# Kernel tuning notes

Measured on AMD Instinct MI355X. Metric: run time of the kernel, lower is better.

Reference implementation:

```python
import jax, jax.numpy as jnp
import numpy as np

B, C, HF, WF = 64, 512, 28, 28
HID = 512
NUM_CLS = 30
LOC_REG = 8
MAX_LEN = 500  # loop runs MAX_LEN + 1 = 501 steps


def setup_inputs() -> dict:
    key = jax.random.key(0)
    ks = jax.random.split(key, 12)
    sc = 0.02
    rn = lambda k, shape: jax.random.normal(k, shape, jnp.float32) * sc
    z = lambda shape: jnp.zeros(shape, jnp.float32)
    return {
        "fea": jax.random.normal(ks[0], (B, C, HF, WF), jnp.float32),
        # AttentionGRUCell params
        "i2h_w": rn(ks[1], (HID, C)),            # Linear(C, H, bias=False)
        "h2h_w": rn(ks[2], (HID, HID)),
        "h2h_b": z((HID,)),
        "score_w": rn(ks[3], (1, HID)),          # Linear(H, 1, bias=False)
        "gru_w_ih": rn(ks[4], (3 * HID, C + NUM_CLS)),
        "gru_w_hh": rn(ks[5], (3 * HID, HID)),
        "gru_b_ih": z((3 * HID,)),
        "gru_b_hh": z((3 * HID,)),
        # structure_generator: Linear(H,H) -> Linear(H, NUM_CLS) (no activation)
        "sg1_w": rn(ks[6], (HID, HID)), "sg1_b": z((HID,)),
        "sg2_w": rn(ks[7], (NUM_CLS, HID)), "sg2_b": z((NUM_CLS,)),
        # loc_generator: Linear(H,H) -> Linear(H, LOC_REG) -> Sigmoid
        "lg1_w": rn(ks[8], (HID, HID)), "lg1_b": z((HID,)),
        "lg2_w": rn(ks[9], (LOC_REG, HID)), "lg2_b": z((LOC_REG,)),
    }


def reference(fea, i2h_w, h2h_w, h2h_b, score_w, gru_w_ih, gru_w_hh,
              gru_b_ih, gru_b_hh, sg1_w, sg1_b, sg2_w, sg2_b,
              lg1_w, lg1_b, lg2_w, lg2_b):
    b = fea.shape[0]
    feat = fea.reshape(b, fea.shape[1], -1).transpose(0, 2, 1)      # [B, T, C]
    # i2h(batch_H) is step-invariant: hoist it out of the decode loop
    feat_proj = jnp.einsum('btc,hc->bth', feat, i2h_w)              # [B, T, H]
    sv = score_w[0]                                                  # [H]

    def gru_cell(x, h):
        gi = x @ gru_w_ih.T + gru_b_ih
        gh = h @ gru_w_hh.T + gru_b_hh
        i_r, i_z, i_n = jnp.split(gi, 3, axis=-1)
        h_r, h_z, h_n = jnp.split(gh, 3, axis=-1)
        r = jax.nn.sigmoid(i_r + h_r)
        z = jax.nn.sigmoid(i_z + h_z)
        n = jnp.tanh(i_n + r * h_n)
        return (1.0 - z) * n + z * h

    def step(carry, _):
        hidden, pre_chars = carry
        onehot = jax.nn.one_hot(pre_chars, NUM_CLS, dtype=feat.dtype)
        hproj = hidden @ h2h_w.T + h2h_b                             # [B, H]
        e = jnp.einsum('bth,h->bt', jnp.tanh(feat_proj + hproj[:, None, :]), sv)
        alpha = jax.nn.softmax(e, axis=1)                            # [B, T]
        context = jnp.einsum('bt,btc->bc', alpha, feat)              # [B, C]
        x = jnp.concatenate([context, onehot], axis=1)               # [B, C+NUM_CLS]
        new_hidden = gru_cell(x, hidden)
        structure_step = (new_hidden @ sg1_w.T + sg1_b) @ sg2_w.T + sg2_b
        loc_step = jax.nn.sigmoid((new_hidden @ lg1_w.T + lg1_b) @ lg2_w.T + lg2_b)
        new_chars = jnp.argmax(structure_step, axis=1)               # greedy decode
        return (new_hidden, new_chars), (structure_step, loc_step)

    hidden0 = jnp.zeros((b, HID), feat.dtype)
    chars0 = jnp.zeros((b,), jnp.int32)
    _, (structs, locs) = jax.lax.scan(step, (hidden0, chars0), None, length=MAX_LEN + 1)
    structure_probs = jax.nn.softmax(structs.transpose(1, 0, 2), axis=-1)  # eval-mode softmax
    loc_preds = locs.transpose(1, 0, 2)
    return structure_probs, loc_preds
```

## Files before the change

### kernel.cpp

```cpp
#include <hip/hip_runtime.h>
#include <hip/hip_bf16.h>


#define NB 64
#define TT 784
#define CC 512
#define HH 512
#define NCLS 30
#define LREG 8
#define STEPS 501
#define GRID_MAIN 256
#define THR_MAIN 1024
#define LROWS 52

struct SlaP {
  __hip_bfloat16* feat16;
  __hip_bfloat16* fp16;
  float* hid2;
  float* hproj;
  float* h1sg;
  float* h1lg;
  float* ctx2;
  float* wsum;
  int*   chars;
  unsigned* bar;
  const float *score_w, *w_ih, *w_hh, *b_ih, *b_hh;
  const float *h2h_w, *h2h_b, *sg1_w, *sg1_b, *sg2_w, *sg2_b;
  const float *lg1_w, *lg1_b, *lg2_w, *lg2_b;
  float *out_probs, *out_loc;
};

__device__ __forceinline__ float lo16(unsigned v){ return __uint_as_float(v << 16); }
__device__ __forceinline__ float hi16(unsigned v){ return __uint_as_float(v & 0xffff0000u); }

__device__ __forceinline__ float cld(const float* p){
  return __hip_atomic_load(p, __ATOMIC_RELAXED, __HIP_MEMORY_SCOPE_AGENT);
}
__device__ __forceinline__ void cst(float* p, float v){
  __hip_atomic_store(p, v, __ATOMIC_RELAXED, __HIP_MEMORY_SCOPE_AGENT);
}
__device__ __forceinline__ int cldi(const int* p){
  return __hip_atomic_load(p, __ATOMIC_RELAXED, __HIP_MEMORY_SCOPE_AGENT);
}
__device__ __forceinline__ void csti(int* p, int v){
  __hip_atomic_store(p, v, __ATOMIC_RELAXED, __HIP_MEMORY_SCOPE_AGENT);
}
__device__ __forceinline__ float2 cld2(const float* p){
  unsigned long long v = __hip_atomic_load((const unsigned long long*)p,
                          __ATOMIC_RELAXED, __HIP_MEMORY_SCOPE_AGENT);
  union { unsigned long long u; float2 f; } c; c.u = v; return c.f;
}
__device__ __forceinline__ void cst2(float* p, float a, float b){
  union { unsigned long long u; float2 f; } c; c.f = make_float2(a, b);
  __hip_atomic_store((unsigned long long*)p, c.u,
                     __ATOMIC_RELAXED, __HIP_MEMORY_SCOPE_AGENT);
}

__device__ __forceinline__ float tanh_fast(float x){
  float ex = __expf(2.f * x);
  return 1.f - 2.f * __builtin_amdgcn_rcpf(ex + 1.f);
}
__device__ __forceinline__ float sigmoid_fast(float x){
  return __builtin_amdgcn_rcpf(1.f + __expf(-x));
}
__device__ __forceinline__ float warp_sum(float v){
  #pragma unroll
  for (int m = 32; m > 0; m >>= 1) v += __shfl_xor(v, m, 64);
  return v;
}
__device__ __forceinline__ float warp_max(float v){
  #pragma unroll
  for (int m = 32; m > 0; m >>= 1) v = fmaxf(v, __shfl_xor(v, m, 64));
  return v;
}
__device__ __forceinline__ int warp_min_i(int v){
  #pragma unroll
  for (int m = 32; m > 0; m >>= 1) v = min(v, __shfl_xor(v, m, 64));
  return v;
}

__device__ __forceinline__ void att_quad(const uint4* f, const uint4* g, int count,
                                         const float* hpr, const float* svr,
                                         float* acc, float& wsr){
  float e[4];
  #pragma unroll
  for (int j = 0; j < 4; ++j){
    float s = 0.f, x;
    x = lo16(f[j].x)+hpr[0]; s += tanh_fast(x)*svr[0];
    x = hi16(f[j].x)+hpr[1]; s += tanh_fast(x)*svr[1];
    x = lo16(f[j].y)+hpr[2]; s += tanh_fast(x)*svr[2];
    x = hi16(f[j].y)+hpr[3]; s += tanh_fast(x)*svr[3];
    x = lo16(f[j].z)+hpr[4]; s += tanh_fast(x)*svr[4];
    x = hi16(f[j].z)+hpr[5]; s += tanh_fast(x)*svr[5];
    x = lo16(f[j].w)+hpr[6]; s += tanh_fast(x)*svr[6];
    x = hi16(f[j].w)+hpr[7]; s += tanh_fast(x)*svr[7];
    e[j] = s;
  }
  #pragma unroll
  for (int m = 32; m > 0; m >>= 1){
    e[0] += __shfl_xor(e[0], m, 64);
    e[1] += __shfl_xor(e[1], m, 64);
    e[2] += __shfl_xor(e[2], m, 64);
    e[3] += __shfl_xor(e[3], m, 64);
  }
  float w[4];
  #pragma unroll
  for (int j = 0; j < 4; ++j) w[j] = (j < count) ? __expf(e[j]) : 0.f;
  #pragma unroll
  for (int j = 0; j < 4; ++j){
    acc[0] += w[j]*lo16(g[j].x); acc[1] += w[j]*hi16(g[j].x);
    acc[2] += w[j]*lo16(g[j].y); acc[3] += w[j]*hi16(g[j].y);
    acc[4] += w[j]*lo16(g[j].z); acc[5] += w[j]*hi16(g[j].z);
    acc[6] += w[j]*lo16(g[j].w); acc[7] += w[j]*hi16(g[j].w);
    wsr += w[j];
  }
}

__device__ __forceinline__ void gbar(unsigned* bar, unsigned target){
  __syncthreads();
  if (threadIdx.x == 0){
    unsigned* c8 = bar + 8 + (blockIdx.x & 7) * 32;
    unsigned p = __hip_atomic_fetch_add(c8, 1u, __ATOMIC_RELAXED, __HIP_MEMORY_SCOPE_AGENT);
    if (p == 32u * target - 1u){
      unsigned pm = __hip_atomic_fetch_add(bar, 1u, __ATOMIC_RELAXED, __HIP_MEMORY_SCOPE_AGENT);
      if (pm == 8u * target - 1u)
        __hip_atomic_store(bar + 64, target, __ATOMIC_RELAXED, __HIP_MEMORY_SCOPE_AGENT);
    }
    while (__hip_atomic_load(bar + 64, __ATOMIC_RELAXED, __HIP_MEMORY_SCOPE_AGENT) < target)
      __builtin_amdgcn_s_sleep(1);
  }
  __syncthreads();
}


__global__ void k_init(SlaP p){
  int idx = blockIdx.x * blockDim.x + threadIdx.x;
  if (idx < 32768){ p.hid2[idx] = 0.f; p.ctx2[idx] = 0.f; }
  if (idx < 64*512) p.hproj[idx] = p.h2h_b[idx & 511];
  if (idx < 64){ p.wsum[idx] = 0.f; p.chars[idx] = 0; }
  if (idx < 512) p.bar[idx] = 0u;
}

__global__ void k_transpose(const float* __restrict__ fea, __hip_bfloat16* __restrict__ feat16){
  __shared__ float tile[64][65];
  const int b = blockIdx.z, t0 = blockIdx.x * 64, c0 = blockIdx.y * 64;
  #pragma unroll
  for (int r = 0; r < 16; ++r){
    int idx = threadIdx.x + 256*r;
    int ci = idx >> 6, tj = idx & 63;
    float v = 0.f;
    if (t0 + tj < TT) v = fea[((size_t)b*CC + (c0+ci))*TT + t0 + tj];
    tile[ci][tj] = v;
  }
  __syncthreads();
  #pragma unroll
  for (int r = 0; r < 16; ++r){
    int idx = threadIdx.x + 256*r;
    int tj = idx >> 6, ci = idx & 63;
    if (t0 + tj < TT)
      feat16[((size_t)b*TT + t0 + tj)*CC + c0 + ci] = __float2bfloat16(tile[ci][tj]);
  }
}

__global__ void k_fpgemm(const float* __restrict__ fea, const float* __restrict__ i2h,
                         __hip_bfloat16* __restrict__ fp16){
  const int b = blockIdx.z, t0 = blockIdx.x * 64, h0 = blockIdx.y * 64;
  const int tx = threadIdx.x & 15, ty = threadIdx.x >> 4;
  const int tb = t0 + tx*4, hb = h0 + ty*4;
  const int ts = (tb < TT) ? tb : 0;
  const float* A = fea + (size_t)b*CC*TT;
  float acc[4][4];
  #pragma unroll
  for (int j = 0; j < 4; ++j)
    #pragma unroll
    for (int i2 = 0; i2 < 4; ++i2) acc[j][i2] = 0.f;
  for (int k = 0; k < CC; ++k){
    const float4 a4 = *(const float4*)&A[(size_t)k*TT + ts];
    float bv0 = i2h[(size_t)(hb+0)*CC + k];
    float bv1 = i2h[(size_t)(hb+1)*CC + k];
    float bv2 = i2h[(size_t)(hb+2)*CC + k];
    float bv3 = i2h[(size_t)(hb+3)*CC + k];
    acc[0][0] += bv0*a4.x; acc[0][1] += bv0*a4.y; acc[0][2] += bv0*a4.z; acc[0][3] += bv0*a4.w;
    acc[1][0] += bv1*a4.x; acc[1][1] += bv1*a4.y; acc[1][2] += bv1*a4.z; acc[1][3] += bv1*a4.w;
    acc[2][0] += bv2*a4.x; acc[2][1] += bv2*a4.y; acc[2][2] += bv2*a4.z; acc[2][3] += bv2*a4.w;
    acc[3][0] += bv3*a4.x; acc[3][1] += bv3*a4.y; acc[3][2] += bv3*a4.z; acc[3][3] += bv3*a4.w;
  }
  if (tb < TT){
    #pragma unroll
    for (int j = 0; j < 4; ++j)
      #pragma unroll
      for (int i2 = 0; i2 < 4; ++i2)
        fp16[((size_t)b*TT + tb + i2)*CC + hb + j] = __float2bfloat16(acc[j][i2]);
  }
}


__global__ void __launch_bounds__(THR_MAIN, 4) sla_main(SlaP p){
  const int tid  = threadIdx.x;
  const int lane = tid & 63;
  const int wv   = tid >> 6;
  const int blk  = blockIdx.x;
  __shared__ float sm[12352];
  __shared__ unsigned short lfp[LROWS*512];
  __shared__ unsigned short lft[LROWS*512];
  float* smF = sm + 12288;

  const int ab = blk >> 2;
  const int aslice = blk & 3;
  float svr[8];
  #pragma unroll
  for (int k = 0; k < 8; ++k) svr[k] = p.score_w[lane*8 + k];

  const int lbase = wv*3 + ((wv < 4) ? wv : 4);
  const int lcnt  = (wv < 4) ? 4 : 3;
  const int gbase = LROWS + wv*9;

  unsigned bid = 0;

  for (int i = 0; i <= STEPS; ++i){
    if (i > 0 && blk < NB){
      const int fb = blk;
      for (int task = wv; task < 38; task += 16){
        const float* wrow; const float* src; float bias;
        if (task < 30){ wrow = p.sg2_w + task*512; bias = p.sg2_b[task]; src = p.h1sg + fb*512; }
        else          { wrow = p.lg2_w + (task-30)*512; bias = p.lg2_b[task-30]; src = p.h1lg + fb*512; }
        float s = 0.f;
        #pragma unroll
        for (int kq = 0; kq < 4; ++kq){
          const float2 wv2 = *(const float2*)&wrow[lane*2 + 128*kq];
          const float2 sv2 = cld2(&src[lane*2 + 128*kq]);
          s += wv2.x*sv2.x + wv2.y*sv2.y;
        }
        s = warp_sum(s);
        if (task < 30){ if (lane == 0) smF[task] = s + bias; }
        else if (lane == 0)
          p.out_loc[(size_t)fb*(STEPS*LREG) + (size_t)(i-1)*LREG + (task-30)] = sigmoid_fast(s + bias);
      }
    }
    __syncthreads();
    if (i > 0 && blk < NB && wv == 0){
      float sv_ = (lane < 30) ? smF[lane] : -3.4e38f;
      float m = warp_max(sv_);
      float e = (lane < 30) ? __expf(sv_ - m) : 0.f;
      float ssum = warp_sum(e);
      if (lane < 30)
        p.out_probs[(size_t)blk*(STEPS*NCLS) + (size_t)(i-1)*NCLS + lane] = e / ssum;
      int cand = (lane < 30 && sv_ == m) ? lane : 1000;
      cand = warp_min_i(cand);
      if (lane == 0) csti(&p.chars[blk], cand);
    }
    if (i == STEPS) break;
    {
      float hpr[8];
      #pragma unroll
      for (int k = 0; k < 4; ++k){
        float2 h2 = cld2(&p.hproj[ab*512 + lane*8 + 2*k]);
        hpr[2*k] = h2.x; hpr[2*k+1] = h2.y;
      }
      float acc[8] = {0,0,0,0,0,0,0,0};
      float wsr = 0.f;
      const int tl0 = aslice * 196;
      const unsigned short* fpB = (const unsigned short*)p.fp16 +
                                  ((size_t)ab*TT + tl0)*512 + lane*8;
      const unsigned short* ftB = (const unsigned short*)p.feat16 +
                                  ((size_t)ab*TT + tl0)*512 + lane*8;
      uint4 qf[2][4], qg[2][4];
      #pragma unroll
      for (int j = 0; j < 4; ++j){
        qf[0][j] = *(const uint4*)(fpB + (size_t)(gbase+j)*512);
        qg[0][j] = *(const uint4*)(ftB + (size_t)(gbase+j)*512);
      }
      #pragma unroll
      for (int j = 0; j < 4; ++j){
        qf[1][j] = *(const uint4*)(fpB + (size_t)(gbase+4+j)*512);
        qg[1][j] = *(const uint4*)(ftB + (size_t)(gbase+4+j)*512);
      }
      {
        uint4 lf[4], lg[4];
        if (i == 0){
          #pragma unroll
          for (int j = 0; j < 4; ++j){
            const int rj = lbase + ((j < lcnt) ? j : (lcnt-1));
            lf[j] = *(const uint4*)(fpB + (size_t)rj*512);
            lg[j] = *(const uint4*)(ftB + (size_t)rj*512);
          }
          #pragma unroll
          for (int j = 0; j < 4; ++j){
            if (j < lcnt){
              *(uint4*)&lfp[(lbase+j)*512 + lane*8] = lf[j];
              *(uint4*)&lft[(lbase+j)*512 + lane*8] = lg[j];
            }
          }
        } else {
          #pragma unroll
          for (int j = 0; j < 4; ++j){
            const int rj = lbase + ((j < lcnt) ? j : (lcnt-1));
            lf[j] = *(const uint4*)&lfp[rj*512 + lane*8];
            lg[j] = *(const uint4*)&lft[rj*512 + lane*8];
          }
        }
        att_quad(lf, lg, lcnt, hpr, svr, acc, wsr);
      }
      att_quad(qf[0], qg[0], 4, hpr, svr, acc, wsr);
      qf[0][0] = *(const uint4*)(fpB + (size_t)(gbase+8)*512);
      qg[0][0] = *(const uint4*)(ftB + (size_t)(gbase+8)*512);
      att_quad(qf[1], qg[1], 4, hpr, svr, acc, wsr);
      att_quad(qf[0], qg[0], 1, hpr, svr, acc, wsr);
      if (wv < 8){
        #pragma unroll
        for (int k = 0; k < 8; ++k) sm[wv*512 + lane*8 + k] = acc[k];
      }
      if (lane == 0) smF[32 + wv] = wsr;
      __syncthreads();
      if (wv >= 8){
        #pragma unroll
        for (int k = 0; k < 8; ++k) sm[(wv-8)*512 + lane*8 + k] += acc[k];
      }
      __syncthreads();
      if (tid < 512){
        float s = 0.f;
        #pragma unroll
        for (int r = 0; r < 8; ++r) s += sm[r*512 + tid];
        unsafeAtomicAdd(&p.ctx2[(tid >> 1)*128 + ab*2 + (tid & 1)], s);
      } else if (tid == 512){
        float s = 0.f;
        #pragma unroll
        for (int r = 0; r < 16; ++r) s += smF[32 + r];
        unsafeAtomicAdd(&p.wsum[ab], s);
      }
    }
    gbar(p.bar, ++bid);
    if (blk < 128){
      const int j0 = blk * 4;
      const float* hidC = p.hid2 + (i & 1)*(512*64);
      float accI[4][3], accH[4][3];
      #pragma unroll
      for (int jj = 0; jj < 4; ++jj)
        #pragma unroll
        for (int g = 0; g < 3; ++g){ accI[jj][g] = 0.f; accH[jj][g] = 0.f; }
      const int kb = wv * 32;
      for (int kk = 0; kk < 32; kk += 4){
        const int k = kb + kk;
        const float2 x01 = cld2(&p.ctx2[(k >> 1)*128 + lane*2]);
        const float2 x23 = cld2(&p.ctx2[(k >> 1)*128 + 128 + lane*2]);
        const float2 h01 = cld2(&hidC[(k >> 1)*128 + lane*2]);
        const float2 h23 = cld2(&hidC[(k >> 1)*128 + 128 + lane*2]);
        #pragma unroll
        for (int jj = 0; jj < 4; ++jj)
          #pragma unroll
          for (int g = 0; g < 3; ++g){
            const int row = g*512 + j0 + jj;
            const float4 wi = *(const float4*)&p.w_ih[(size_t)row*542 + k];
            const float4 wh = *(const float4*)&p.w_hh[(size_t)row*512 + k];
            accI[jj][g] += wi.x*x01.x + wi.y*x01.y + wi.z*x23.x + wi.w*x23.y;
            accH[jj][g] += wh.x*h01.x + wh.y*h01.y + wh.z*h23.x + wh.w*h23.y;
          }
      }
      const int slot = wv & 7;
      if (wv < 8){
        #pragma unroll
        for (int jj = 0; jj < 4; ++jj)
          #pragma unroll
          for (int g = 0; g < 3; ++g){
            sm[((slot*24) + jj*6 + g    )*64 + lane] = accI[jj][g];
            sm[((slot*24) + jj*6 + 3 + g)*64 + lane] = accH[jj][g];
          }
      }
      __syncthreads();
      if (wv >= 8){
        #pragma unroll
        for (int jj = 0; jj < 4; ++jj)
          #pragma unroll
          for (int g = 0; g < 3; ++g){
            sm[((slot*24) + jj*6 + g    )*64 + lane] += accI[jj][g];
            sm[((slot*24) + jj*6 + 3 + g)*64 + lane] += accH[jj][g];
          }
      }
      __syncthreads();
      if (tid < 128){
        const int pp = tid >> 6;
        const int b = tid & 63;
        const float inv = 1.f / cld(&p.wsum[b]);
        const int ch = cldi(&p.chars[b]);
        const float2 ho = cld2(&hidC[((j0 >> 1) + pp)*128 + b*2]);
        float nh[2];
        #pragma unroll
        for (int q = 0; q < 2; ++q){
          const int jj = pp*2 + q;
          float gi[3], gh[3];
          #pragma unroll
          for (int g = 0; g < 3; ++g){
            float giS = 0.f, ghS = 0.f;
            #pragma unroll
            for (int sl = 0; sl < 8; ++sl){
              giS += sm[((sl*24) + jj*6 + g    )*64 + b];
              ghS += sm[((sl*24) + jj*6 + 3 + g)*64 + b];
            }
            const int row = g*512 + j0 + jj;
            gi[g] = giS*inv + p.w_ih[(size_t)row*542 + 512 + ch] + p.b_ih[row];
            gh[g] = ghS + p.b_hh[row];
          }
          float r_ = sigmoid_fast(gi[0] + gh[0]);
          float z_ = sigmoid_fast(gi[1] + gh[1]);
          float n_ = tanh_fast(gi[2] + r_*gh[2]);
          float hold = (q == 0) ? ho.x : ho.y;
          nh[q] = (1.f - z_)*n_ + z_*hold;
        }
        cst2(&p.hid2[((i+1) & 1)*(512*64) + ((j0 >> 1) + pp)*128 + b*2], nh[0], nh[1]);
      }
    } else {
      __syncthreads(); __syncthreads();
    }
    gbar(p.bar, ++bid);
    if (blk < 128){
      const int r0 = blk * 12;
      const float* hidN = p.hid2 + ((i+1) & 1)*(512*64);
      const float* rowp[12];
      #pragma unroll
      for (int r = 0; r < 12; ++r){
        const int rg = r0 + r, head = rg >> 9, j = rg & 511;
        const float* base = (head == 0) ? p.h2h_w : (head == 1) ? p.sg1_w : p.lg1_w;
        rowp[r] = base + (size_t)j*512;
      }
      float acc[12];
      #pragma unroll
      for (int r = 0; r < 12; ++r) acc[r] = 0.f;
      const int kb = wv * 32;
      for (int kk = 0; kk < 32; kk += 4){
        const int k = kb + kk;
        const float2 h01 = cld2(&hidN[(k >> 1)*128 + lane*2]);
        const float2 h23 = cld2(&hidN[(k >> 1)*128 + 128 + lane*2]);
        #pragma unroll
        for (int r = 0; r < 12; ++r){
          const float4 w4 = *(const float4*)&rowp[r][k];
          acc[r] += w4.x*h01.x + w4.y*h01.y + w4.z*h23.x + w4.w*h23.y;
        }
      }
      const int slot = wv & 7;
      if (wv < 8){
        #pragma unroll
        for (int r = 0; r < 12; ++r) sm[((slot*12) + r)*64 + lane] = acc[r];
      }
      __syncthreads();
      if (wv >= 8){
        #pragma unroll
        for (int r = 0; r < 12; ++r) sm[((slot*12) + r)*64 + lane] += acc[r];
      }
      __syncthreads();
      if (tid < 384){
        const int q = tid >> 6, b = tid & 63;
        float s0 = 0.f, s1 = 0.f;
        #pragma unroll
        for (int sl = 0; sl < 8; ++sl){
          s0 += sm[((sl*12) + 2*q    )*64 + b];
          s1 += sm[((sl*12) + 2*q + 1)*64 + b];
        }
        const int rg = r0 + 2*q, head = rg >> 9, j = rg & 511;
        const float* bb = (head == 0) ? p.h2h_b : (head == 1) ? p.sg1_b : p.lg1_b;
        float* dst = (head == 0) ? p.hproj : (head == 1) ? p.h1sg : p.h1lg;
        cst2(&dst[b*512 + j], s0 + bb[j], s1 + bb[j+1]);
      }
    } else {
      const int bz = blk - 128;
      if (tid < 256) cst(&p.ctx2[bz*256 + tid], 0.f);
      if (bz == 127 && tid < 64) cst(&p.wsum[tid], 0.f);
      __syncthreads(); __syncthreads();
    }
    gbar(p.bar, ++bid);
  }
}

extern "C" void kernel_launch(void* const* d_in, const int* in_sizes, int n_in,
                              void* d_out, int out_size, void* d_ws, size_t ws_size,
                              hipStream_t stream){
  (void)in_sizes; (void)n_in; (void)out_size; (void)ws_size;
  char* w = (char*)d_ws;
  size_t off = 0;
  auto carve = [&](size_t bytes) -> char* {
    char* r = w + off; off += (bytes + 255) & ~(size_t)255; return r;
  };
  SlaP p;
  p.feat16 = (__hip_bfloat16*)carve((size_t)NB*TT*CC*2);
  p.fp16   = (__hip_bfloat16*)carve((size_t)NB*TT*HH*2);
  p.hid2   = (float*)carve((size_t)2*512*64*4);
  p.hproj  = (float*)carve((size_t)64*512*4);
  p.h1sg   = (float*)carve((size_t)64*512*4);
  p.h1lg   = (float*)carve((size_t)64*512*4);
  p.ctx2   = (float*)carve((size_t)512*64*4);
  p.wsum   = (float*)carve(64*4);
  p.chars  = (int*)carve(64*4);
  p.bar    = (unsigned*)carve(2048);

  p.score_w = (const float*)d_in[4];
  p.w_ih  = (const float*)d_in[5];  p.w_hh  = (const float*)d_in[6];
  p.b_ih  = (const float*)d_in[7];  p.b_hh  = (const float*)d_in[8];
  p.h2h_w = (const float*)d_in[2];  p.h2h_b = (const float*)d_in[3];
  p.sg1_w = (const float*)d_in[9];  p.sg1_b = (const float*)d_in[10];
  p.sg2_w = (const float*)d_in[11]; p.sg2_b = (const float*)d_in[12];
  p.lg1_w = (const float*)d_in[13]; p.lg1_b = (const float*)d_in[14];
  p.lg2_w = (const float*)d_in[15]; p.lg2_b = (const float*)d_in[16];
  p.out_probs = (float*)d_out;
  p.out_loc   = p.out_probs + (size_t)NB*STEPS*NCLS;

  const float* fea = (const float*)d_in[0];
  const float* i2h = (const float*)d_in[1];

  k_init<<<128, 256, 0, stream>>>(p);
  k_transpose<<<dim3(13, 8, 64), 256, 0, stream>>>(fea, p.feat16);
  k_fpgemm<<<dim3(13, 8, 64), 256, 0, stream>>>(fea, i2h, p.fp16);
  sla_main<<<GRID_MAIN, THR_MAIN, 0, stream>>>(p);
}
```

Before: 46.41 ms.

## Store projected features in FP8 fully in LDS; stream bf16 features with alternating order

The step-invariant feature projection is now stored as FP8 instead of bf16. This lets each block's whole 196-row slice fit in shared memory, loaded once at step 0, so every attention step reads projections only from LDS. The bf16 context features are streamed from global memory each step through a 4-deep register prefetch, and the traversal direction flips on alternate steps to improve cache reuse. The attention scores are now computed for all rows first, then weighted and accumulated. This reduces per-step global traffic, at the cost of FP8 quantization error in the attention scores.

```diff
diff --git a/kernel.cpp b/kernel.cpp
--- a/kernel.cpp
+++ b/kernel.cpp
@@ -11,11 +11,12 @@
 #define STEPS 501
 #define GRID_MAIN 256
 #define THR_MAIN 1024
-#define LROWS 52
+
+typedef float floatx2 __attribute__((ext_vector_type(2)));
 
 struct SlaP {
   __hip_bfloat16* feat16;
-  __hip_bfloat16* fp16;
+  unsigned char* scr8;
   float* hid2;
   float* hproj;
   float* h1sg;
@@ -79,43 +80,6 @@
   return v;
 }
 
-__device__ __forceinline__ void att_quad(const uint4* f, const uint4* g, int count,
-                                         const float* hpr, const float* svr,
-                                         float* acc, float& wsr){
-  float e[4];
-  #pragma unroll
-  for (int j = 0; j < 4; ++j){
-    float s = 0.f, x;
-    x = lo16(f[j].x)+hpr[0]; s += tanh_fast(x)*svr[0];
-    x = hi16(f[j].x)+hpr[1]; s += tanh_fast(x)*svr[1];
-    x = lo16(f[j].y)+hpr[2]; s += tanh_fast(x)*svr[2];
-    x = hi16(f[j].y)+hpr[3]; s += tanh_fast(x)*svr[3];
-    x = lo16(f[j].z)+hpr[4]; s += tanh_fast(x)*svr[4];
-    x = hi16(f[j].z)+hpr[5]; s += tanh_fast(x)*svr[5];
-    x = lo16(f[j].w)+hpr[6]; s += tanh_fast(x)*svr[6];
-    x = hi16(f[j].w)+hpr[7]; s += tanh_fast(x)*svr[7];
-    e[j] = s;
-  }
-  #pragma unroll
-  for (int m = 32; m > 0; m >>= 1){
-    e[0] += __shfl_xor(e[0], m, 64);
-    e[1] += __shfl_xor(e[1], m, 64);
-    e[2] += __shfl_xor(e[2], m, 64);
-    e[3] += __shfl_xor(e[3], m, 64);
-  }
-  float w[4];
-  #pragma unroll
-  for (int j = 0; j < 4; ++j) w[j] = (j < count) ? __expf(e[j]) : 0.f;
-  #pragma unroll
-  for (int j = 0; j < 4; ++j){
-    acc[0] += w[j]*lo16(g[j].x); acc[1] += w[j]*hi16(g[j].x);
-    acc[2] += w[j]*lo16(g[j].y); acc[3] += w[j]*hi16(g[j].y);
-    acc[4] += w[j]*lo16(g[j].z); acc[5] += w[j]*hi16(g[j].z);
-    acc[6] += w[j]*lo16(g[j].w); acc[7] += w[j]*hi16(g[j].w);
-    wsr += w[j];
-  }
-}
-
 __device__ __forceinline__ void gbar(unsigned* bar, unsigned target){
   __syncthreads();
   if (threadIdx.x == 0){
@@ -163,7 +127,7 @@
 }
 
 __global__ void k_fpgemm(const float* __restrict__ fea, const float* __restrict__ i2h,
-                         __hip_bfloat16* __restrict__ fp16){
+                         unsigned char* __restrict__ scr8){
   const int b = blockIdx.z, t0 = blockIdx.x * 64, h0 = blockIdx.y * 64;
   const int tx = threadIdx.x & 15, ty = threadIdx.x >> 4;
   const int tb = t0 + tx*4, hb = h0 + ty*4;
@@ -187,10 +151,11 @@
   }
   if (tb < TT){
     #pragma unroll
-    for (int j = 0; j < 4; ++j)
-      #pragma unroll
-      for (int i2 = 0; i2 < 4; ++i2)
-        fp16[((size_t)b*TT + tb + i2)*CC + hb + j] = __float2bfloat16(acc[j][i2]);
+    for (int i2 = 0; i2 < 4; ++i2){
+      int pk = __builtin_amdgcn_cvt_pk_fp8_f32(acc[0][i2], acc[1][i2], 0, false);
+      pk = __builtin_amdgcn_cvt_pk_fp8_f32(acc[2][i2], acc[3][i2], pk, true);
+      *(int*)&scr8[((size_t)b*TT + tb + i2)*512 + hb] = pk;
+    }
   }
 }
 
@@ -201,8 +166,8 @@
   const int wv   = tid >> 6;
   const int blk  = blockIdx.x;
   __shared__ float sm[12352];
-  __shared__ unsigned short lfp[LROWS*512];
-  __shared__ unsigned short lft[LROWS*512];
+  __shared__ uint4 lsc4[6272];
+  unsigned char* lsc = (unsigned char*)lsc4;
   float* smF = sm + 12288;
 
   const int ab = blk >> 2;
@@ -211,9 +176,8 @@
   #pragma unroll
   for (int k = 0; k < 8; ++k) svr[k] = p.score_w[lane*8 + k];
 
-  const int lbase = wv*3 + ((wv < 4) ? wv : 4);
-  const int lcnt  = (wv < 4) ? 4 : 3;
-  const int gbase = LROWS + wv*9;
+  const int cnt = (wv < 4) ? 13 : 12;
+  const int r0r = wv*12 + ((wv < 4) ? wv : 4);
 
   unsigned bid = 0;
 
@@ -250,6 +214,11 @@
       if (lane == 0) csti(&p.chars[blk], cand);
     }
     if (i == STEPS) break;
+    if (i == 0){
+      const uint4* g = (const uint4*)(p.scr8 + ((size_t)ab*TT + aslice*196)*512);
+      for (int idx = tid; idx < 6272; idx += THR_MAIN) lsc4[idx] = g[idx];
+      __syncthreads();
+    }
     {
       float hpr[8];
       #pragma unroll
@@ -257,55 +226,65 @@
         float2 h2 = cld2(&p.hproj[ab*512 + lane*8 + 2*k]);
         hpr[2*k] = h2.x; hpr[2*k+1] = h2.y;
       }
+      float e[13];
+      #pragma unroll
+      for (int r = 0; r < 13; ++r){
+        if (r < cnt){
+          const uint2 rd = *(const uint2*)&lsc[(r0r + r)*512 + lane*8];
+          const floatx2 p01 = __builtin_amdgcn_cvt_pk_f32_fp8(rd.x, false);
+          const floatx2 p23 = __builtin_amdgcn_cvt_pk_f32_fp8(rd.x, true);
+          const floatx2 p45 = __builtin_amdgcn_cvt_pk_f32_fp8(rd.y, false);
+          const floatx2 p67 = __builtin_amdgcn_cvt_pk_f32_fp8(rd.y, true);
+          float s = 0.f;
+          s += tanh_fast(p01.x + hpr[0]) * svr[0];
+          s += tanh_fast(p01.y + hpr[1]) * svr[1];
+          s += tanh_fast(p23.x + hpr[2]) * svr[2];
+          s += tanh_fast(p23.y + hpr[3]) * svr[3];
+          s += tanh_fast(p45.x + hpr[4]) * svr[4];
+          s += tanh_fast(p45.y + hpr[5]) * svr[5];
+          s += tanh_fast(p67.x + hpr[6]) * svr[6];
+          s += tanh_fast(p67.y + hpr[7]) * svr[7];
+          e[r] = s;
+        } else e[r] = 0.f;
+      }
+      #pragma unroll
+      for (int m = 32; m > 0; m >>= 1){
+        #pragma unroll
+        for (int r = 0; r < 13; ++r) e[r] += __shfl_xor(e[r], m, 64);
+      }
+      float w[13];
+      float wsr = 0.f;
+      #pragma unroll
+      for (int r = 0; r < 13; ++r){
+        if (r < cnt){ w[r] = __expf(e[r]); wsr += w[r]; }
+        else w[r] = 0.f;
+      }
+      const int fwd = ((i & 1) == 0);
+      const unsigned short* ftB = (const unsigned short*)p.feat16 +
+                                  ((size_t)ab*TT + aslice*196)*512 + lane*8;
       float acc[8] = {0,0,0,0,0,0,0,0};
-      float wsr = 0.f;
-      const int tl0 = aslice * 196;
-      const unsigned short* fpB = (const unsigned short*)p.fp16 +
-                                  ((size_t)ab*TT + tl0)*512 + lane*8;
-      const unsigned short* ftB = (const unsigned short*)p.feat16 +
-                                  ((size_t)ab*TT + tl0)*512 + lane*8;
-      uint4 qf[2][4], qg[2][4];
+      uint4 buf[4];
       #pragma unroll
       for (int j = 0; j < 4; ++j){
-        qf[0][j] = *(const uint4*)(fpB + (size_t)(gbase+j)*512);
-        qg[0][j] = *(const uint4*)(ftB + (size_t)(gbase+j)*512);
-      }
-      #pragma unroll
-      for (int j = 0; j < 4; ++j){
-        qf[1][j] = *(const uint4*)(fpB + (size_t)(gbase+4+j)*512);
-        qg[1][j] = *(const uint4*)(ftB + (size_t)(gbase+4+j)*512);
-      }
-      {
-        uint4 lf[4], lg[4];
-        if (i == 0){
-          #pragma unroll
-          for (int j = 0; j < 4; ++j){
-            const int rj = lbase + ((j < lcnt) ? j : (lcnt-1));
-            lf[j] = *(const uint4*)(fpB + (size_t)rj*512);
-            lg[j] = *(const uint4*)(ftB + (size_t)rj*512);
+        const int row = fwd ? (r0r + j) : (r0r + cnt - 1 - j);
+        buf[j] = *(const uint4*)(ftB + (size_t)row*512);
+      }
+      #pragma unroll
+      for (int r = 0; r < 13; ++r){
+        if (r < cnt){
+          const uint4 ct = buf[r & 3];
+          if (r + 4 < cnt){
+            const int row = fwd ? (r0r + r + 4) : (r0r + cnt - 1 - (r + 4));
+            buf[r & 3] = *(const uint4*)(ftB + (size_t)row*512);
           }
-          #pragma unroll
-          for (int j = 0; j < 4; ++j){
-            if (j < lcnt){
-              *(uint4*)&lfp[(lbase+j)*512 + lane*8] = lf[j];
-              *(uint4*)&lft[(lbase+j)*512 + lane*8] = lg[j];
-            }
-          }
-        } else {
-          #pragma unroll
-          for (int j = 0; j < 4; ++j){
-            const int rj = lbase + ((j < lcnt) ? j : (lcnt-1));
-            lf[j] = *(const uint4*)&lfp[rj*512 + lane*8];
-            lg[j] = *(const uint4*)&lft[rj*512 + lane*8];
-          }
+          const int ri = fwd ? r : (cnt - 1 - r);
+          const float wg = w[ri];
+          acc[0] += wg*lo16(ct.x); acc[1] += wg*hi16(ct.x);
+          acc[2] += wg*lo16(ct.y); acc[3] += wg*hi16(ct.y);
+          acc[4] += wg*lo16(ct.z); acc[5] += wg*hi16(ct.z);
+          acc[6] += wg*lo16(ct.w); acc[7] += wg*hi16(ct.w);
         }
-        att_quad(lf, lg, lcnt, hpr, svr, acc, wsr);
-      }
-      att_quad(qf[0], qg[0], 4, hpr, svr, acc, wsr);
-      qf[0][0] = *(const uint4*)(fpB + (size_t)(gbase+8)*512);
-      qg[0][0] = *(const uint4*)(ftB + (size_t)(gbase+8)*512);
-      att_quad(qf[1], qg[1], 4, hpr, svr, acc, wsr);
-      att_quad(qf[0], qg[0], 1, hpr, svr, acc, wsr);
+      }
       if (wv < 8){
         #pragma unroll
         for (int k = 0; k < 8; ++k) sm[wv*512 + lane*8 + k] = acc[k];
@@ -481,7 +460,7 @@
   };
   SlaP p;
   p.feat16 = (__hip_bfloat16*)carve((size_t)NB*TT*CC*2);
-  p.fp16   = (__hip_bfloat16*)carve((size_t)NB*TT*HH*2);
+  p.scr8   = (unsigned char*)carve((size_t)NB*TT*HH);
   p.hid2   = (float*)carve((size_t)2*512*64*4);
   p.hproj  = (float*)carve((size_t)64*512*4);
   p.h1sg   = (float*)carve((size_t)64*512*4);
@@ -507,6 +486,6 @@
 
   k_init<<<128, 256, 0, stream>>>(p);
   k_transpose<<<dim3(13, 8, 64), 256, 0, stream>>>(fea, p.feat16);
-  k_fpgemm<<<dim3(13, 8, 64), 256, 0, stream>>>(fea, i2h, p.fp16);
+  k_fpgemm<<<dim3(13, 8, 64), 256, 0, stream>>>(fea, i2h, p.scr8);
   sla_main<<<GRID_MAIN, THR_MAIN, 0, stream>>>(p);
 }
```

Result: faster. 42.34 ms (-8.8%).
